# Optimization experiments

Measured on AMD Instinct MI355X. Metric: run time of the kernel, lower is better.

Reference implementation:

```python
import jax, jax.numpy as jnp
import numpy as np

N_HASHES = 4
CHUNK = 144
REDUCTION = 4
RES_SCALE = 0.1
L2_EPS = 5e-5


def _conv(x, w, b):
    # keras Conv2D, strides 1, padding 'same', NHWC/HWIO
    return jax.lax.conv_general_dilated(
        x, w, window_strides=(1, 1), padding='SAME',
        dimension_numbers=('NHWC', 'HWIO', 'NHWC')) + b


def setup_inputs() -> dict:
    key = jax.random.key(0)
    ks = jax.random.split(key, 4)
    N, H, W, Ch = 4, 96, 96, 256
    C = Ch // REDUCTION
    hb = min((H * W) // CHUNK + ((H * W) // CHUNK) % 2, 128)  # = 64
    return {
        'input': jax.random.normal(ks[0], (N, H, W, Ch), jnp.float32),
        'w_match': jax.random.normal(ks[1], (3, 3, Ch, C), jnp.float32) * 0.02,
        'b_match': jnp.zeros((C,), jnp.float32),
        'w_asm': jax.random.normal(ks[2], (3, 3, Ch, Ch), jnp.float32) * 0.02,
        'b_asm': jnp.zeros((Ch,), jnp.float32),
        'rotations': jax.random.normal(ks[3], (C, N_HASHES, hb // 2), jnp.float32),
    }


def reference(input, w_match, b_match, w_asm, b_asm, rotations):
    N, H, W, Ch = input.shape
    L = H * W
    C = Ch // REDUCTION
    nh = N_HASHES

    xm = _conv(input, w_match, b_match)   # (N,H,W,C)
    ya = _conv(input, w_asm, b_asm)       # (N,H,W,Ch)
    # Faithful to the TF code: reshape NHWC buffer to (N, C, L) then transpose.
    x_embed = xm.reshape(N, -1, L).transpose(0, 2, 1)  # (N, L, C)
    y_embed = ya.reshape(N, -1, L).transpose(0, 2, 1)  # (N, L, Ch)

    hash_buckets = min(L // CHUNK + (L // CHUNK) % 2, 128)
    # LSH: random rotations shared across batch
    rot = jnp.einsum('btf,fhi->bhti', x_embed, rotations)       # (N,nh,L,hb/2)
    rot = jnp.concatenate([rot, -rot], axis=-1)                 # (N,nh,L,hb)
    codes = jnp.argmax(rot, axis=-1).astype(jnp.int32)          # (N,nh,L)
    codes = codes + (jnp.arange(nh, dtype=jnp.int32) * hash_buckets)[None, :, None]
    codes = codes.reshape(N, -1)                                # (N, nh*L)

    idx = jnp.argsort(codes, axis=-1)
    undo_sort = jnp.argsort(idx, axis=-1)
    mod = idx % L

    xs = jnp.take_along_axis(x_embed, mod[..., None], axis=1)   # (N, nh*L, C)
    ys = jnp.take_along_axis(y_embed, mod[..., None], axis=1)   # (N, nh*L, Ch)

    pad = (CHUNK - L % CHUNK) % CHUNK
    xb = xs.reshape(N, nh, L, C)
    yb = ys.reshape(N, nh, L, Ch)
    if pad:
        xb = jnp.concatenate([xb, xb[:, :, -pad:]], axis=2)
        yb = jnp.concatenate([yb, yb[:, :, -pad:]], axis=2)
    xb = xb.reshape(N, nh, -1, CHUNK, C)    # (N,nh,K,chunk,C)
    yb = yb.reshape(N, nh, -1, CHUNK, Ch)

    # tf.math.l2_normalize: x * rsqrt(max(sum(x^2), eps))
    ss = jnp.sum(xb * xb, axis=-1, keepdims=True)
    x_match = xb * jax.lax.rsqrt(jnp.maximum(ss, L2_EPS))

    def add_adjacent(t):  # concat bucket, bucket-1, bucket+1 along chunk axis
        return jnp.concatenate(
            [t, jnp.roll(t, 1, axis=2), jnp.roll(t, -1, axis=2)], axis=3)

    x_match = add_adjacent(x_match)         # (N,nh,K,3*chunk,C)
    y3 = add_adjacent(yb)                   # (N,nh,K,3*chunk,Ch)

    raw = jnp.einsum('bhkie,bhkje->bhkij', xb, x_match)  # (N,nh,K,chunk,3chunk)
    lse = jax.scipy.special.logsumexp(raw, axis=-1, keepdims=True)
    score = jnp.exp(raw - lse)
    ret = jnp.einsum('bhkij,bhkje->bhkie', score, y3)    # (N,nh,K,chunk,Ch)

    ret = ret.reshape(N, nh, -1, Ch)
    bs = lse.reshape(N, nh, -1)
    if pad:
        ret = ret[:, :, :-pad]
        bs = bs[:, :, :-pad]

    ret = ret.reshape(N, nh * L, Ch)
    bs = bs.reshape(N, nh * L)
    ret = jnp.take_along_axis(ret, undo_sort[..., None], axis=1)
    bs = jnp.take_along_axis(bs, undo_sort, axis=1)

    ret = ret.reshape(N, nh, L, Ch)
    probs = jax.nn.softmax(bs.reshape(N, nh, L, 1), axis=1)
    ret = jnp.sum(ret * probs, axis=1)      # (N, L, Ch)

    ret = ret.transpose(0, 2, 1).reshape(N, H, W, Ch)  # inverse of the TF reshape
    return ret * RES_SCALE + input
```

## Files before the change

kernel.cpp:

```cpp
#include <hip/hip_runtime.h>
#include <cstdint>
#include <cstddef>

#define NB 4
#define HH 96
#define WW 96
#define CHN 256
#define CC 64
#define LL 9216
#define NHASH 4
#define HBK 64
#define CHK 144
#define NCHUNK 64
#define NJ 36864

typedef __attribute__((ext_vector_type(8))) short bf16x8;
typedef __attribute__((ext_vector_type(8))) unsigned short u16x8;
typedef __attribute__((ext_vector_type(4))) float f32x4;

__device__ __forceinline__ unsigned short f2b(float f) {
    unsigned int x = __float_as_uint(f);
    x += 0x7FFFu + ((x >> 16) & 1u);
    return (unsigned short)(x >> 16);
}
__device__ __forceinline__ float b2f(unsigned short u) {
    return __uint_as_float(((unsigned int)u) << 16);
}

__global__ __launch_bounds__(256) void cvt_in_hilo_k(const float* __restrict__ in,
                                                     unsigned short* __restrict__ hi,
                                                     unsigned short* __restrict__ lo)
{
    size_t g = ((size_t)blockIdx.x * 256 + threadIdx.x) * 8;
    float4 v0 = *(const float4*)(in + g);
    float4 v1 = *(const float4*)(in + g + 4);
    float xs[8] = {v0.x, v0.y, v0.z, v0.w, v1.x, v1.y, v1.z, v1.w};
    u16x8 h, l;
#pragma unroll
    for (int i = 0; i < 8; i++) {
        unsigned short hv = f2b(xs[i]);
        h[i] = hv;
        l[i] = f2b(xs[i] - b2f(hv));
    }
    *(u16x8*)(hi + g) = h;
    *(u16x8*)(lo + g) = l;
}

__global__ __launch_bounds__(256) void cvt_wm_hilo_k(const float* __restrict__ w,
                                                     unsigned short* __restrict__ hiT,
                                                     unsigned short* __restrict__ loT)
{
    __shared__ float tl[32][33];
    const int tap = blockIdx.z;
    const int c0 = blockIdx.x * 32;
    const int o0 = blockIdx.y * 32;
    const int tx = threadIdx.x & 31, ty0 = threadIdx.x >> 5;
#pragma unroll
    for (int i = 0; i < 32; i += 8)
        tl[ty0 + i][tx] = w[((size_t)tap * 256 + c0 + ty0 + i) * 64 + o0 + tx];
    __syncthreads();
#pragma unroll
    for (int i = 0; i < 32; i += 8) {
        float v = tl[tx][ty0 + i];
        unsigned short h = f2b(v);
        size_t o = ((size_t)tap * 64 + o0 + ty0 + i) * 256 + c0 + tx;
        hiT[o] = h;
        loT[o] = f2b(v - b2f(h));
    }
}

#define ASTR2 72
__global__ __launch_bounds__(256, 2) void conv_match_mfma_k(
    const unsigned short* __restrict__ in_hi, const unsigned short* __restrict__ in_lo,
    const unsigned short* __restrict__ wmT_hi, const unsigned short* __restrict__ wmT_lo,
    const float* __restrict__ bias, float* __restrict__ xm)
{
    __shared__ short Ah[64 * ASTR2], Al[64 * ASTR2];
    __shared__ short Bh[64 * ASTR2], Bl[64 * ASTR2];
    const int n = blockIdx.z, p0 = blockIdx.x * 64;
    const int tid = threadIdx.x;
    const int w = tid >> 6;
    const int lane = tid & 63, lm = lane & 15, lq = lane >> 4;
    const int r = tid >> 2, q8 = (tid & 3) * 8;
    const int p = p0 + r, py = p / WW, px = p % WW;
    const unsigned short* hiN = in_hi + (size_t)n * LL * CHN;
    const unsigned short* loN = in_lo + (size_t)n * LL * CHN;

    f32x4 acc[4];
#pragma unroll
    for (int b = 0; b < 4; b++) acc[b] = (f32x4){0.f, 0.f, 0.f, 0.f};

    u16x8 avh0 = (u16x8){0,0,0,0,0,0,0,0}, avh1 = (u16x8){0,0,0,0,0,0,0,0};
    u16x8 avl0 = (u16x8){0,0,0,0,0,0,0,0}, avl1 = (u16x8){0,0,0,0,0,0,0,0};
    u16x8 bvh0, bvh1, bvl0, bvl1;
    {
        int sy = py - 1, sx = px - 1;
        if (((unsigned)sy < HH) && ((unsigned)sx < WW)) {
            size_t ao = (size_t)(sy * WW + sx) * CHN + q8;
            avh0 = *(const u16x8*)(hiN + ao);
            avh1 = *(const u16x8*)(hiN + ao + 32);
            avl0 = *(const u16x8*)(loN + ao);
            avl1 = *(const u16x8*)(loN + ao + 32);
        }
        size_t bo = (size_t)r * 256 + q8;
        bvh0 = *(const u16x8*)(wmT_hi + bo);
        bvh1 = *(const u16x8*)(wmT_hi + bo + 32);
        bvl0 = *(const u16x8*)(wmT_lo + bo);
        bvl1 = *(const u16x8*)(wmT_lo + bo + 32);
    }

#pragma unroll 1
    for (int it = 0; it < 36; it++) {
        __syncthreads();
        *(u16x8*)&Ah[r * ASTR2 + q8]      = avh0;
        *(u16x8*)&Ah[r * ASTR2 + q8 + 32] = avh1;
        *(u16x8*)&Al[r * ASTR2 + q8]      = avl0;
        *(u16x8*)&Al[r * ASTR2 + q8 + 32] = avl1;
        *(u16x8*)&Bh[r * ASTR2 + q8]      = bvh0;
        *(u16x8*)&Bh[r * ASTR2 + q8 + 32] = bvh1;
        *(u16x8*)&Bl[r * ASTR2 + q8]      = bvl0;
        *(u16x8*)&Bl[r * ASTR2 + q8 + 32] = bvl1;
        if (it < 35) {
            int nit = it + 1;
            int ntap = nit >> 2, nci = (nit & 3) << 6;
            int ky = ntap / 3, kx = ntap - ky * 3;
            int sy = py + ky - 1, sx = px + kx - 1;
            avh0 = (u16x8){0,0,0,0,0,0,0,0}; avh1 = (u16x8){0,0,0,0,0,0,0,0};
            avl0 = (u16x8){0,0,0,0,0,0,0,0}; avl1 = (u16x8){0,0,0,0,0,0,0,0};
            if (((unsigned)sy < HH) && ((unsigned)sx < WW)) {
                size_t ao = (size_t)(sy * WW + sx) * CHN + q8 + nci;
                avh0 = *(const u16x8*)(hiN + ao);
                avh1 = *(const u16x8*)(hiN + ao + 32);
                avl0 = *(const u16x8*)(loN + ao);
                avl1 = *(const u16x8*)(loN + ao + 32);
            }
            size_t bo = ((size_t)ntap * 64 + r) * 256 + q8 + nci;
            bvh0 = *(const u16x8*)(wmT_hi + bo);
            bvh1 = *(const u16x8*)(wmT_hi + bo + 32);
            bvl0 = *(const u16x8*)(wmT_lo + bo);
            bvl1 = *(const u16x8*)(wmT_lo + bo + 32);
        }
        __syncthreads();
#pragma unroll
        for (int cs = 0; cs < 2; cs++) {
            bf16x8 afh = *(const bf16x8*)&Ah[(w * 16 + lm) * ASTR2 + cs * 32 + lq * 8];
            bf16x8 afl = *(const bf16x8*)&Al[(w * 16 + lm) * ASTR2 + cs * 32 + lq * 8];
#pragma unroll
            for (int nt = 0; nt < 4; nt++) {
                bf16x8 bfh = *(const bf16x8*)&Bh[(nt * 16 + lm) * ASTR2 + cs * 32 + lq * 8];
                bf16x8 bfl = *(const bf16x8*)&Bl[(nt * 16 + lm) * ASTR2 + cs * 32 + lq * 8];
                acc[nt] = __builtin_amdgcn_mfma_f32_16x16x32_bf16(afh, bfh, acc[nt], 0, 0, 0);
                acc[nt] = __builtin_amdgcn_mfma_f32_16x16x32_bf16(afh, bfl, acc[nt], 0, 0, 0);
                acc[nt] = __builtin_amdgcn_mfma_f32_16x16x32_bf16(afl, bfh, acc[nt], 0, 0, 0);
            }
        }
    }
    float bvv[4];
#pragma unroll
    for (int nt = 0; nt < 4; nt++) bvv[nt] = bias[nt * 16 + lm];
    float* outN = xm + (size_t)n * LL * 64;
#pragma unroll
    for (int r4 = 0; r4 < 4; r4++) {
        int row = p0 + w * 16 + lq * 4 + r4;
        float* od = outN + (size_t)row * 64;
#pragma unroll
        for (int nt = 0; nt < 4; nt++)
            od[nt * 16 + lm] = acc[nt][r4] + bvv[nt];
    }
}

__global__ __launch_bounds__(256) void transpose_k(const float* __restrict__ in, float* __restrict__ out,
                                                   unsigned short* __restrict__ out_bf, int R, int Cc)
{
    __shared__ float tl[32][33];
    const int n = blockIdx.z;
    const size_t base = (size_t)n * R * Cc;
    int c0 = blockIdx.x * 32, r0 = blockIdx.y * 32;
    int tx = threadIdx.x & 31, ty0 = threadIdx.x >> 5;
#pragma unroll
    for (int i = 0; i < 32; i += 8)
        tl[ty0 + i][tx] = in[base + (size_t)(r0 + ty0 + i) * Cc + c0 + tx];
    __syncthreads();
#pragma unroll
    for (int i = 0; i < 32; i += 8) {
        float v = tl[tx][ty0 + i];
        size_t o = base + (size_t)(c0 + ty0 + i) * R + r0 + tx;
        out[o] = v;
        out_bf[o] = f2b(v);
    }
}

__global__ __launch_bounds__(256) void cvt_wT_k(const float* __restrict__ w, unsigned short* __restrict__ wT)
{
    __shared__ float tl[32][33];
    const int tap = blockIdx.z;
    const int c0 = blockIdx.x * 32;
    const int o0 = blockIdx.y * 32;
    const int tx = threadIdx.x & 31, ty0 = threadIdx.x >> 5;
#pragma unroll
    for (int i = 0; i < 32; i += 8)
        tl[ty0 + i][tx] = w[((size_t)tap * 256 + c0 + ty0 + i) * 256 + o0 + tx];
    __syncthreads();
#pragma unroll
    for (int i = 0; i < 32; i += 8)
        wT[((size_t)tap * 256 + o0 + ty0 + i) * 256 + c0 + tx] = f2b(tl[tx][ty0 + i]);
}

__global__ __launch_bounds__(256) void conv_mfma_k(
    const unsigned short* __restrict__ in_bf, const unsigned short* __restrict__ wT,
    const float* __restrict__ bias, unsigned short* __restrict__ ya_bf)
{
    __shared__ short As[128 * ASTR2];
    __shared__ short Bs[128 * ASTR2];
    const int n = blockIdx.z, p0 = blockIdx.x * 128, co0 = blockIdx.y * 128;
    const int tid = threadIdx.x;
    const int w = tid >> 6, wr = w >> 1, wc = w & 1;
    const int lane = tid & 63, lm = lane & 15, lq = lane >> 4;
    const int r = tid >> 1, hf = tid & 1;
    const int p = p0 + r, py = p / WW, px = p % WW;
    const unsigned short* inN = in_bf + (size_t)n * LL * CHN;

    f32x4 acc[4][4];
#pragma unroll
    for (int a = 0; a < 4; a++)
#pragma unroll
        for (int b = 0; b < 4; b++) acc[a][b] = (f32x4){0.f, 0.f, 0.f, 0.f};

    u16x8 av0 = (u16x8){0,0,0,0,0,0,0,0}, av1 = (u16x8){0,0,0,0,0,0,0,0};
    u16x8 av2 = (u16x8){0,0,0,0,0,0,0,0}, av3 = (u16x8){0,0,0,0,0,0,0,0};
    u16x8 bv0, bv1, bv2, bv3;
    {
        int sy = py - 1, sx = px - 1;
        if (((unsigned)sy < HH) && ((unsigned)sx < WW)) {
            const unsigned short* asrc = inN + (size_t)(sy * WW + sx) * CHN + hf * 32;
            av0 = *(const u16x8*)(asrc);
            av1 = *(const u16x8*)(asrc + 8);
            av2 = *(const u16x8*)(asrc + 16);
            av3 = *(const u16x8*)(asrc + 24);
        }
        const unsigned short* bsrc = wT + ((size_t)co0 + r) * 256 + hf * 32;
        bv0 = *(const u16x8*)(bsrc);
        bv1 = *(const u16x8*)(bsrc + 8);
        bv2 = *(const u16x8*)(bsrc + 16);
        bv3 = *(const u16x8*)(bsrc + 24);
    }

#pragma unroll 1
    for (int it = 0; it < 36; it++) {
        __syncthreads();
        *(u16x8*)&As[r * ASTR2 + hf * 32]      = av0;
        *(u16x8*)&As[r * ASTR2 + hf * 32 + 8]  = av1;
        *(u16x8*)&As[r * ASTR2 + hf * 32 + 16] = av2;
        *(u16x8*)&As[r * ASTR2 + hf * 32 + 24] = av3;
        *(u16x8*)&Bs[r * ASTR2 + hf * 32]      = bv0;
        *(u16x8*)&Bs[r * ASTR2 + hf * 32 + 8]  = bv1;
        *(u16x8*)&Bs[r * ASTR2 + hf * 32 + 16] = bv2;
        *(u16x8*)&Bs[r * ASTR2 + hf * 32 + 24] = bv3;
        if (it < 35) {
            int nit = it + 1;
            int ntap = nit >> 2, nci = (nit & 3) << 6;
            int ky = ntap / 3, kx = ntap - ky * 3;
            int sy = py + ky - 1, sx = px + kx - 1;
            av0 = (u16x8){0,0,0,0,0,0,0,0}; av1 = (u16x8){0,0,0,0,0,0,0,0};
            av2 = (u16x8){0,0,0,0,0,0,0,0}; av3 = (u16x8){0,0,0,0,0,0,0,0};
            if (((unsigned)sy < HH) && ((unsigned)sx < WW)) {
                const unsigned short* asrc = inN + (size_t)(sy * WW + sx) * CHN + hf * 32 + nci;
                av0 = *(const u16x8*)(asrc);
                av1 = *(const u16x8*)(asrc + 8);
                av2 = *(const u16x8*)(asrc + 16);
                av3 = *(const u16x8*)(asrc + 24);
            }
            const unsigned short* bsrc = wT + ((size_t)ntap * 256 + co0 + r) * 256 + hf * 32 + nci;
            bv0 = *(const u16x8*)(bsrc);
            bv1 = *(const u16x8*)(bsrc + 8);
            bv2 = *(const u16x8*)(bsrc + 16);
            bv3 = *(const u16x8*)(bsrc + 24);
        }
        __syncthreads();
#pragma unroll
        for (int cs = 0; cs < 2; cs++) {
            bf16x8 af[4], bf[4];
#pragma unroll
            for (int mt = 0; mt < 4; mt++)
                af[mt] = *(const bf16x8*)&As[(wr * 64 + mt * 16 + lm) * ASTR2 + cs * 32 + lq * 8];
#pragma unroll
            for (int nt = 0; nt < 4; nt++)
                bf[nt] = *(const bf16x8*)&Bs[(wc * 64 + nt * 16 + lm) * ASTR2 + cs * 32 + lq * 8];
#pragma unroll
            for (int mt = 0; mt < 4; mt++)
#pragma unroll
                for (int nt = 0; nt < 4; nt++)
                    acc[mt][nt] = __builtin_amdgcn_mfma_f32_16x16x32_bf16(af[mt], bf[nt], acc[mt][nt], 0, 0, 0);
        }
    }
    float bv[4];
#pragma unroll
    for (int nt = 0; nt < 4; nt++) bv[nt] = bias[co0 + wc * 64 + nt * 16 + lm];
#pragma unroll
    for (int mt = 0; mt < 4; mt++) {
#pragma unroll
        for (int r4 = 0; r4 < 4; r4++) {
            int row = p0 + wr * 64 + mt * 16 + lq * 4 + r4;
            unsigned short* od = ya_bf + ((size_t)n * LL + row) * CHN + co0 + wc * 64;
#pragma unroll
            for (int nt = 0; nt < 4; nt++)
                od[nt * 16 + lm] = f2b(acc[mt][nt][r4] + bv[nt]);
        }
    }
}

__global__ __launch_bounds__(256) void transpose_bf_k(const unsigned short* __restrict__ in,
                                                      unsigned short* __restrict__ out)
{
    __shared__ unsigned short tl[64][65];
    const int n = blockIdx.z;
    const size_t base = (size_t)n * LL * CHN;
    const int t0 = blockIdx.x * 64, e0 = blockIdx.y * 64;
    const int tx = threadIdx.x & 63, ty0 = threadIdx.x >> 6;
#pragma unroll
    for (int i = 0; i < 16; i++) {
        int row = ty0 + i * 4;
        tl[row][tx] = in[base + (size_t)(e0 + row) * LL + t0 + tx];
    }
    __syncthreads();
#pragma unroll
    for (int i = 0; i < 16; i++) {
        int row = ty0 + i * 4;
        out[base + (size_t)(t0 + row) * CHN + e0 + tx] = tl[tx][row];
    }
}

__global__ __launch_bounds__(256) void hash_k(const float* __restrict__ xmT, const float* __restrict__ rot,
                                              int* __restrict__ codes, float* __restrict__ ssq)
{
    __shared__ float rs[32 * 68];
    const int h = blockIdx.y;
    for (int e = threadIdx.x; e < 2048; e += 256) {
        int hi = e >> 6, f = e & 63;
        rs[hi * 68 + f] = rot[f * 128 + h * 32 + hi];
    }
    __syncthreads();
    int g = blockIdx.x * 256 + threadIdx.x;
    int n = g / LL, t = g % LL;
    float4 x4[16];
    const float* src = xmT + (size_t)g * CC;
#pragma unroll
    for (int f4 = 0; f4 < 16; f4++) x4[f4] = *(const float4*)(src + f4 * 4);
    if (h == 0) {
        float ss = 0.f;
#pragma unroll
        for (int f4 = 0; f4 < 16; f4++)
            ss += x4[f4].x * x4[f4].x + x4[f4].y * x4[f4].y + x4[f4].z * x4[f4].z + x4[f4].w * x4[f4].w;
        ssq[g] = ss;
    }
    float bp = -1e30f, bn = -1e30f;
    int ip = 0, inn = 0;
    for (int i = 0; i < 32; i++) {
        const float* rr = &rs[i * 68];
        float d0 = 0.f, d1 = 0.f, d2 = 0.f, d3 = 0.f;
#pragma unroll
        for (int f4 = 0; f4 < 16; f4++) {
            float4 r4 = *(const float4*)(rr + f4 * 4);
            d0 = fmaf(x4[f4].x, r4.x, d0);
            d1 = fmaf(x4[f4].y, r4.y, d1);
            d2 = fmaf(x4[f4].z, r4.z, d2);
            d3 = fmaf(x4[f4].w, r4.w, d3);
        }
        float d = (d0 + d1) + (d2 + d3);
        if (d > bp) { bp = d; ip = i; }
        if (-d > bn) { bn = -d; inn = i; }
    }
    int code = (bp >= bn) ? ip : (32 + inn);
    codes[(size_t)n * NJ + h * LL + t] = code + h * HBK;
}

__global__ __launch_bounds__(256) void sort_hist_k(const int* __restrict__ codes, int* __restrict__ hist,
                                                   int* __restrict__ rank)
{
    __shared__ int lhw[4][256];
    const int n = blockIdx.y, seg = blockIdx.x, tid = threadIdx.x;
    const int w = tid >> 6, lane = tid & 63;
    int j = seg * 256 + tid;
    int c = codes[(size_t)n * NJ + j];
    for (int e = tid; e < 1024; e += 256) ((int*)lhw)[e] = 0;
    __syncthreads();
    unsigned long long eq = ~0ull;
#pragma unroll
    for (int b = 0; b < 8; b++) {
        unsigned long long m = __ballot((c >> b) & 1);
        eq &= ((c >> b) & 1) ? m : ~m;
    }
    int rw = __popcll(eq & ((1ull << lane) - 1ull));
    int cntw = __popcll(eq);
    if (rw == 0) lhw[w][c] = cntw;
    __syncthreads();
    int base = 0;
    if (w > 0) base += lhw[0][c];
    if (w > 1) base += lhw[1][c];
    if (w > 2) base += lhw[2][c];
    rank[(size_t)n * NJ + j] = base + rw;
    hist[(size_t)n * NJ + tid * 144 + seg] = lhw[0][tid] + lhw[1][tid] + lhw[2][tid] + lhw[3][tid];
}

__global__ __launch_bounds__(256) void sort_scan_k(int* __restrict__ hist)
{
    const int n = blockIdx.x;
    const int key = threadIdx.x;
    int* hn = hist + (size_t)n * NJ;
    int sum = 0;
    for (int s = 0; s < 144; s++) sum += hn[key * 144 + s];
    __shared__ int sc[256];
    sc[key] = sum;
    __syncthreads();
    for (int off = 1; off < 256; off <<= 1) {
        int v = (key >= off) ? sc[key - off] : 0;
        __syncthreads();
        sc[key] += v;
        __syncthreads();
    }
    int run = sc[key] - sum;
    for (int s = 0; s < 144; s++) { int v = hn[key * 144 + s]; hn[key * 144 + s] = run; run += v; }
}

__global__ __launch_bounds__(256) void sort_scatter_k(const int* __restrict__ codes, const int* __restrict__ rank,
                                                      const int* __restrict__ hist, int* __restrict__ sidx,
                                                      int* __restrict__ undo)
{
    const int n = blockIdx.y, seg = blockIdx.x, tid = threadIdx.x;
    int j = seg * 256 + tid;
    int c = codes[(size_t)n * NJ + j];
    int dest = hist[(size_t)n * NJ + c * 144 + seg] + rank[(size_t)n * NJ + j];
    sidx[(size_t)n * NJ + dest] = j;
    undo[(size_t)n * NJ + j] = dest;
}

#define QSTR 72
#define PSTR 164
__global__ __launch_bounds__(1024, 4) __attribute__((amdgpu_waves_per_eu(4, 4))) void attn_mfma_k(
    const unsigned short* __restrict__ xmT_bf, const unsigned short* __restrict__ yaT,
    const float* __restrict__ ssq, const int* __restrict__ sidx,
    unsigned short* __restrict__ Osort, float* __restrict__ bs)
{
    __shared__ short Qs[144 * QSTR];
    __shared__ short Ks[144 * QSTR];
    __shared__ short Ps[144 * PSTR];
    __shared__ int   tIdx[432];
    __shared__ int   voff[432];
    __shared__ float nfs[432];
    __shared__ float qlen[432];
    __shared__ float lsum[144];
    __shared__ float linv[144];

    const int k = blockIdx.x, h = blockIdx.y, n = blockIdx.z;
    const int tid = threadIdx.x;
    const int w = tid >> 6, lane = tid & 63;
    const int lm = lane & 15, lq = lane >> 4;
    const size_t sbase = (size_t)n * NJ + (size_t)h * LL;

    if (tid < 432) {
        int cc = tid / CHK, rr = tid - cc * CHK;
        int c = (cc == 0) ? k : (cc == 1 ? (k + NCHUNK - 1) & (NCHUNK - 1) : (k + 1) & (NCHUNK - 1));
        int j = sidx[sbase + c * CHK + rr];
        int t = j % LL;
        tIdx[tid] = t;
        voff[tid] = t * (CHN * 2);
        float m = fmaxf(ssq[(size_t)n * LL + t], 5e-5f);
        float nf = rsqrtf(m);
        nfs[tid] = nf;
        qlen[tid] = m * nf;
    }
    __syncthreads();

    const int sr = tid >> 3, sj = (tid & 7) * 8;
    const int sr2 = (tid + 1024) >> 3, sj2 = (tid & 7) * 8;
    {
        u16x8 v = *(const u16x8*)(xmT_bf + ((size_t)n * LL + tIdx[sr]) * CC + sj);
        *(u16x8*)&Qs[sr * QSTR + sj] = v;
        if (tid < 128) {
            u16x8 v2 = *(const u16x8*)(xmT_bf + ((size_t)n * LL + tIdx[sr2]) * CC + sj2);
            *(u16x8*)&Qs[sr2 * QSTR + sj2] = v2;
        }
    }
    for (int e = tid; e < 2304; e += 1024) {
        int r = e >> 4, c = 144 + (e & 15);
        Ps[r * PSTR + c] = 0;
    }
    u16x8 kreg0, kreg1;
    kreg0 = *(const u16x8*)(xmT_bf + ((size_t)n * LL + tIdx[CHK + sr]) * CC + sj);
    if (tid < 128)
        kreg1 = *(const u16x8*)(xmT_bf + ((size_t)n * LL + tIdx[CHK + sr2]) * CC + sj2);

    const char* vbase = (const char*)(yaT + (size_t)n * LL * CHN + w * 16 + lm);
    f32x4 accO[9];
#pragma unroll
    for (int mt = 0; mt < 9; mt++) accO[mt] = (f32x4){0.f, 0.f, 0.f, 0.f};
    f32x4 accL = (f32x4){0.f, 0.f, 0.f, 0.f};
    bf16x8 onesF, onesL;
#pragma unroll
    for (int i = 0; i < 8; i++) {
        onesF[i] = (short)0x3F80;
        onesL[i] = (lq < 2) ? (short)0x3F80 : (short)0;
    }

    for (int cc = 0; cc < 3; cc++) {
        const int c144 = cc * CHK;
        if (cc > 0) {
            *(u16x8*)&Ks[sr * QSTR + sj] = kreg0;
            if (tid < 128) *(u16x8*)&Ks[sr2 * QSTR + sj2] = kreg1;
        }
        if (cc < 2) {
            kreg0 = *(const u16x8*)(xmT_bf + ((size_t)n * LL + tIdx[(cc + 1) * CHK + sr]) * CC + sj);
            if (tid < 128)
                kreg1 = *(const u16x8*)(xmT_bf + ((size_t)n * LL + tIdx[(cc + 1) * CHK + sr2]) * CC + sj2);
        }
        bf16x8 vfrag[5];
#pragma unroll
        for (int ks = 0; ks < 5; ks++) {
            int kb = ks * 32 + lq * 8;
            if (kb < 144) {
                int4 o0 = *(const int4*)&voff[c144 + kb];
                int4 o1 = *(const int4*)&voff[c144 + kb + 4];
                vfrag[ks][0] = (short)*(const unsigned short*)(vbase + o0.x);
                vfrag[ks][1] = (short)*(const unsigned short*)(vbase + o0.y);
                vfrag[ks][2] = (short)*(const unsigned short*)(vbase + o0.z);
                vfrag[ks][3] = (short)*(const unsigned short*)(vbase + o0.w);
                vfrag[ks][4] = (short)*(const unsigned short*)(vbase + o1.x);
                vfrag[ks][5] = (short)*(const unsigned short*)(vbase + o1.y);
                vfrag[ks][6] = (short)*(const unsigned short*)(vbase + o1.z);
                vfrag[ks][7] = (short)*(const unsigned short*)(vbase + o1.w);
            } else {
                vfrag[ks] = (bf16x8){0, 0, 0, 0, 0, 0, 0, 0};
            }
        }
        __syncthreads();

        const short* Bsrc = (cc == 0) ? Qs : Ks;
        for (int tt = w; tt < 81; tt += 16) {
            int mt = tt / 9, nt = tt - mt * 9;
            f32x4 c = {0.f, 0.f, 0.f, 0.f};
#pragma unroll
            for (int ks = 0; ks < 2; ks++) {
                bf16x8 a = *(const bf16x8*)&Qs[(mt * 16 + lm) * QSTR + ks * 32 + lq * 8];
                bf16x8 b = *(const bf16x8*)&Bsrc[(nt * 16 + lm) * QSTR + ks * 32 + lq * 8];
                c = __builtin_amdgcn_mfma_f32_16x16x32_bf16(a, b, c, 0, 0, 0);
            }
            float nfk = nfs[c144 + nt * 16 + lm];
#pragma unroll
            for (int r = 0; r < 4; r++) {
                int mrow = mt * 16 + lq * 4 + r;
                float p = __expf(fmaf(c[r], nfk, -qlen[mrow]));
                Ps[mrow * PSTR + nt * 16 + lm] = (short)f2b(p);
            }
        }
        __syncthreads();

        if (w < 9) {
#pragma unroll
            for (int ks = 0; ks < 5; ks++) {
                bf16x8 a = *(const bf16x8*)&Ps[(w * 16 + lm) * PSTR + ks * 32 + lq * 8];
                accL = __builtin_amdgcn_mfma_f32_16x16x32_bf16(a, (ks == 4) ? onesL : onesF, accL, 0, 0, 0);
            }
        }
#pragma unroll
        for (int mt = 0; mt < 9; mt++) {
            f32x4 c = accO[mt];
#pragma unroll
            for (int ks = 0; ks < 5; ks++) {
                bf16x8 a = *(const bf16x8*)&Ps[(mt * 16 + lm) * PSTR + ks * 32 + lq * 8];
                c = __builtin_amdgcn_mfma_f32_16x16x32_bf16(a, vfrag[ks], c, 0, 0, 0);
            }
            accO[mt] = c;
        }
    }

    if (w < 9 && lm == 0) {
#pragma unroll
        for (int r = 0; r < 4; r++) lsum[w * 16 + lq * 4 + r] = accL[r];
    }
    __syncthreads();
    if (tid < 144) {
        float l = lsum[tid];
        linv[tid] = 1.0f / l;
        bs[sbase + tIdx[tid]] = qlen[tid] + __logf(l);
    }
    __syncthreads();

#pragma unroll
    for (int mt = 0; mt < 9; mt++) {
        f32x4 c = accO[mt];
#pragma unroll
        for (int r = 0; r < 4; r++) {
            int mrow = mt * 16 + lq * 4 + r;
            Osort[(sbase + (size_t)k * CHK + mrow) * CHN + w * 16 + lm] = f2b(c[r] * linv[mrow]);
        }
    }
}

__global__ __launch_bounds__(256) void combfin_k(
    const unsigned short* __restrict__ Osort, const float* __restrict__ bs,
    const int* __restrict__ undo, const float* __restrict__ inp, float* __restrict__ out)
{
    __shared__ float ac[32][260];
    __shared__ int   uS[4][32];
    __shared__ float pS[4][32];
    const int n = blockIdx.y;
    const int t0 = blockIdx.x * 32;
    const int tid = threadIdx.x;
    if (tid < 128) {
        int hh = tid >> 5, tt = tid & 31;
        size_t idx = (size_t)n * NJ + (size_t)hh * LL + t0 + tt;
        uS[hh][tt] = undo[idx];
        pS[hh][tt] = bs[idx];
    }
    __syncthreads();
    if (tid < 32) {
        float b0 = pS[0][tid], b1 = pS[1][tid], b2 = pS[2][tid], b3 = pS[3][tid];
        float mx = fmaxf(fmaxf(b0, b1), fmaxf(b2, b3));
        float e0 = __expf(b0 - mx), e1 = __expf(b1 - mx), e2 = __expf(b2 - mx), e3 = __expf(b3 - mx);
        float inv = 1.f / (e0 + e1 + e2 + e3);
        pS[0][tid] = e0 * inv; pS[1][tid] = e1 * inv; pS[2][tid] = e2 * inv; pS[3][tid] = e3 * inv;
    }
    __syncthreads();
    const int g = tid & 63, tq = tid >> 6;
    for (int tt8 = 0; tt8 < 8; tt8++) {
        int t = tq * 8 + tt8;
        float a0 = 0.f, a1 = 0.f, a2 = 0.f, a3 = 0.f;
#pragma unroll
        for (int hh = 0; hh < 4; hh++) {
            int row = uS[hh][t];
            float p = pS[hh][t];
            ushort4 u = *(const ushort4*)&Osort[((size_t)n * NJ + row) * CHN + g * 4];
            a0 = fmaf(p, b2f(u.x), a0);
            a1 = fmaf(p, b2f(u.y), a1);
            a2 = fmaf(p, b2f(u.z), a2);
            a3 = fmaf(p, b2f(u.w), a3);
        }
        *(float4*)&ac[t][g * 4] = make_float4(a0, a1, a2, a3);
    }
    __syncthreads();
    const int tp = tid & 31, er = tid >> 5;
    const float* inN = inp + (size_t)n * LL * CHN;
    float* outN = out + (size_t)n * LL * CHN;
    for (int it = 0; it < 32; it++) {
        int e = er + it * 8;
        size_t o = (size_t)e * LL + t0 + tp;
        outN[o] = ac[tp][e] * 0.1f + inN[o];
    }
}

extern "C" void kernel_launch(void* const* d_in, const int* in_sizes, int n_in,
                              void* d_out, int out_size, void* d_ws, size_t ws_size,
                              hipStream_t stream)
{
    (void)in_sizes; (void)n_in; (void)out_size; (void)ws_size;
    const float* input   = (const float*)d_in[0];
    const float* w_match = (const float*)d_in[1];
    const float* b_match = (const float*)d_in[2];
    const float* w_asm   = (const float*)d_in[3];
    const float* b_asm   = (const float*)d_in[4];
    const float* rot     = (const float*)d_in[5];
    float* out = (float*)d_out;

    char* ws = (char*)d_ws;
    size_t off = 0;
    auto alloc = [&](size_t bytes) -> void* {
        void* p = ws + off;
        off += (bytes + 255) & ~(size_t)255;
        return p;
    };
    unsigned short* in_bf  = (unsigned short*)alloc((size_t)NB * LL * CHN * 2);
    unsigned short* wT_bf  = (unsigned short*)alloc((size_t)9 * CHN * CHN * 2);
    unsigned short* ya_bf  = (unsigned short*)alloc((size_t)NB * LL * CHN * 2);
    unsigned short* yaT    = (unsigned short*)alloc((size_t)NB * LL * CHN * 2);
    float* xm     = (float*)alloc((size_t)NB * LL * CC * 4);
    float* xmT    = (float*)alloc((size_t)NB * LL * CC * 4);
    unsigned short* xmT_bf = (unsigned short*)alloc((size_t)NB * LL * CC * 2);
    float* ssq    = (float*)alloc((size_t)NB * LL * 4);
    int*   codes  = (int*)  alloc((size_t)NB * NJ * 4);
    int*   rank   = (int*)  alloc((size_t)NB * NJ * 4);
    int*   hist   = (int*)  alloc((size_t)NB * NJ * 4);
    int*   sidx   = (int*)  alloc((size_t)NB * NJ * 4);
    int*   undo   = (int*)  alloc((size_t)NB * NJ * 4);
    float* bs     = (float*)alloc((size_t)NB * NJ * 4);
    unsigned short* Osort = (unsigned short*)alloc((size_t)NB * NJ * CHN * 2);
    unsigned short* wmT_hi = (unsigned short*)alloc((size_t)9 * 64 * CHN * 2);
    unsigned short* wmT_lo = (unsigned short*)alloc((size_t)9 * 64 * CHN * 2);
    unsigned short* in_lo = Osort;

    cvt_in_hilo_k<<<dim3(4608), 256, 0, stream>>>(input, in_bf, in_lo);
    cvt_wm_hilo_k<<<dim3(8, 2, 9), 256, 0, stream>>>(w_match, wmT_hi, wmT_lo);
    conv_match_mfma_k<<<dim3(144, 1, NB), 256, 0, stream>>>(in_bf, in_lo, wmT_hi, wmT_lo, b_match, xm);
    transpose_k<<<dim3(288, 2, NB), 256, 0, stream>>>(xm, xmT, xmT_bf, CC, LL);
    cvt_wT_k<<<dim3(8, 8, 9), 256, 0, stream>>>(w_asm, wT_bf);
    conv_mfma_k<<<dim3(72, 2, NB), 256, 0, stream>>>(in_bf, wT_bf, b_asm, ya_bf);
    transpose_bf_k<<<dim3(144, 4, NB), 256, 0, stream>>>(ya_bf, yaT);
    hash_k<<<dim3(144, NHASH), 256, 0, stream>>>(xmT, rot, codes, ssq);
    sort_hist_k<<<dim3(144, NB), 256, 0, stream>>>(codes, hist, rank);
    sort_scan_k<<<dim3(NB), 256, 0, stream>>>(hist);
    sort_scatter_k<<<dim3(144, NB), 256, 0, stream>>>(codes, rank, hist, sidx, undo);
    attn_mfma_k<<<dim3(NCHUNK, NHASH, NB), 1024, 0, stream>>>(xmT_bf, yaT, ssq, sidx, Osort, bs);
    combfin_k<<<dim3(288, NB), 256, 0, stream>>>(Osort, bs, undo, input, out);
}
```

Baseline: 433.8 us.

## Merge independent conv, weight-convert and transpose kernels into combined launches

Combines the two weight-conversion kernels, the match and assembly convolutions, and the two transpose kernels into three launches that split work by block index. This cuts launch count and lets the small match-conv grid share the GPU with the larger assembly conv instead of running alone. In exchange, both branches share one shared-memory and register footprint and the launch bound of 2 blocks per CU. That may lower occupancy for the assembly-conv path, and the two branches have uneven block durations.

```diff
diff --git a/kernel.cpp b/kernel.cpp
--- a/kernel.cpp
+++ b/kernel.cpp
@@ -46,287 +46,291 @@
     *(u16x8*)(lo + g) = l;
 }
 
-__global__ __launch_bounds__(256) void cvt_wm_hilo_k(const float* __restrict__ w,
-                                                     unsigned short* __restrict__ hiT,
-                                                     unsigned short* __restrict__ loT)
+__global__ __launch_bounds__(256) void cvt_w_fused_k(const float* __restrict__ wm,
+                                                     unsigned short* __restrict__ wmT_hi,
+                                                     unsigned short* __restrict__ wmT_lo,
+                                                     const float* __restrict__ wa,
+                                                     unsigned short* __restrict__ wT)
 {
     __shared__ float tl[32][33];
     const int tap = blockIdx.z;
     const int c0 = blockIdx.x * 32;
-    const int o0 = blockIdx.y * 32;
     const int tx = threadIdx.x & 31, ty0 = threadIdx.x >> 5;
-#pragma unroll
-    for (int i = 0; i < 32; i += 8)
-        tl[ty0 + i][tx] = w[((size_t)tap * 256 + c0 + ty0 + i) * 64 + o0 + tx];
-    __syncthreads();
-#pragma unroll
-    for (int i = 0; i < 32; i += 8) {
-        float v = tl[tx][ty0 + i];
-        unsigned short h = f2b(v);
-        size_t o = ((size_t)tap * 64 + o0 + ty0 + i) * 256 + c0 + tx;
-        hiT[o] = h;
-        loT[o] = f2b(v - b2f(h));
+    if (blockIdx.y < 2) {
+        const int o0 = blockIdx.y * 32;
+#pragma unroll
+        for (int i = 0; i < 32; i += 8)
+            tl[ty0 + i][tx] = wm[((size_t)tap * 256 + c0 + ty0 + i) * 64 + o0 + tx];
+        __syncthreads();
+#pragma unroll
+        for (int i = 0; i < 32; i += 8) {
+            float v = tl[tx][ty0 + i];
+            unsigned short h = f2b(v);
+            size_t o = ((size_t)tap * 64 + o0 + ty0 + i) * 256 + c0 + tx;
+            wmT_hi[o] = h;
+            wmT_lo[o] = f2b(v - b2f(h));
+        }
+    } else {
+        const int o0 = (blockIdx.y - 2) * 32;
+#pragma unroll
+        for (int i = 0; i < 32; i += 8)
+            tl[ty0 + i][tx] = wa[((size_t)tap * 256 + c0 + ty0 + i) * 256 + o0 + tx];
+        __syncthreads();
+#pragma unroll
+        for (int i = 0; i < 32; i += 8)
+            wT[((size_t)tap * 256 + o0 + ty0 + i) * 256 + c0 + tx] = f2b(tl[tx][ty0 + i]);
     }
 }
 
 #define ASTR2 72
-__global__ __launch_bounds__(256, 2) void conv_match_mfma_k(
+__global__ __launch_bounds__(256, 2) void convs_fused_k(
     const unsigned short* __restrict__ in_hi, const unsigned short* __restrict__ in_lo,
     const unsigned short* __restrict__ wmT_hi, const unsigned short* __restrict__ wmT_lo,
-    const float* __restrict__ bias, float* __restrict__ xm)
-{
-    __shared__ short Ah[64 * ASTR2], Al[64 * ASTR2];
-    __shared__ short Bh[64 * ASTR2], Bl[64 * ASTR2];
-    const int n = blockIdx.z, p0 = blockIdx.x * 64;
+    const float* __restrict__ b_match, float* __restrict__ xm,
+    const unsigned short* __restrict__ wT, const float* __restrict__ b_asm,
+    unsigned short* __restrict__ ya_bf)
+{
+    __shared__ short smem[256 * ASTR2];
+    const int n = blockIdx.y;
     const int tid = threadIdx.x;
     const int w = tid >> 6;
     const int lane = tid & 63, lm = lane & 15, lq = lane >> 4;
-    const int r = tid >> 2, q8 = (tid & 3) * 8;
-    const int p = p0 + r, py = p / WW, px = p % WW;
-    const unsigned short* hiN = in_hi + (size_t)n * LL * CHN;
-    const unsigned short* loN = in_lo + (size_t)n * LL * CHN;
-
-    f32x4 acc[4];
-#pragma unroll
-    for (int b = 0; b < 4; b++) acc[b] = (f32x4){0.f, 0.f, 0.f, 0.f};
-
-    u16x8 avh0 = (u16x8){0,0,0,0,0,0,0,0}, avh1 = (u16x8){0,0,0,0,0,0,0,0};
-    u16x8 avl0 = (u16x8){0,0,0,0,0,0,0,0}, avl1 = (u16x8){0,0,0,0,0,0,0,0};
-    u16x8 bvh0, bvh1, bvl0, bvl1;
-    {
-        int sy = py - 1, sx = px - 1;
-        if (((unsigned)sy < HH) && ((unsigned)sx < WW)) {
-            size_t ao = (size_t)(sy * WW + sx) * CHN + q8;
-            avh0 = *(const u16x8*)(hiN + ao);
-            avh1 = *(const u16x8*)(hiN + ao + 32);
-            avl0 = *(const u16x8*)(loN + ao);
-            avl1 = *(const u16x8*)(loN + ao + 32);
-        }
-        size_t bo = (size_t)r * 256 + q8;
-        bvh0 = *(const u16x8*)(wmT_hi + bo);
-        bvh1 = *(const u16x8*)(wmT_hi + bo + 32);
-        bvl0 = *(const u16x8*)(wmT_lo + bo);
-        bvl1 = *(const u16x8*)(wmT_lo + bo + 32);
-    }
-
-#pragma unroll 1
-    for (int it = 0; it < 36; it++) {
-        __syncthreads();
-        *(u16x8*)&Ah[r * ASTR2 + q8]      = avh0;
-        *(u16x8*)&Ah[r * ASTR2 + q8 + 32] = avh1;
-        *(u16x8*)&Al[r * ASTR2 + q8]      = avl0;
-        *(u16x8*)&Al[r * ASTR2 + q8 + 32] = avl1;
-        *(u16x8*)&Bh[r * ASTR2 + q8]      = bvh0;
-        *(u16x8*)&Bh[r * ASTR2 + q8 + 32] = bvh1;
-        *(u16x8*)&Bl[r * ASTR2 + q8]      = bvl0;
-        *(u16x8*)&Bl[r * ASTR2 + q8 + 32] = bvl1;
-        if (it < 35) {
-            int nit = it + 1;
-            int ntap = nit >> 2, nci = (nit & 3) << 6;
-            int ky = ntap / 3, kx = ntap - ky * 3;
-            int sy = py + ky - 1, sx = px + kx - 1;
-            avh0 = (u16x8){0,0,0,0,0,0,0,0}; avh1 = (u16x8){0,0,0,0,0,0,0,0};
-            avl0 = (u16x8){0,0,0,0,0,0,0,0}; avl1 = (u16x8){0,0,0,0,0,0,0,0};
+
+    if (blockIdx.x < 144) {
+        short* Ah = smem;
+        short* Al = smem + 64 * ASTR2;
+        short* Bh = smem + 128 * ASTR2;
+        short* Bl = smem + 192 * ASTR2;
+        const int p0 = blockIdx.x * 64;
+        const int r = tid >> 2, q8 = (tid & 3) * 8;
+        const int p = p0 + r, py = p / WW, px = p % WW;
+        const unsigned short* hiN = in_hi + (size_t)n * LL * CHN;
+        const unsigned short* loN = in_lo + (size_t)n * LL * CHN;
+
+        f32x4 acc[4];
+#pragma unroll
+        for (int b = 0; b < 4; b++) acc[b] = (f32x4){0.f, 0.f, 0.f, 0.f};
+
+        u16x8 avh0 = (u16x8){0,0,0,0,0,0,0,0}, avh1 = (u16x8){0,0,0,0,0,0,0,0};
+        u16x8 avl0 = (u16x8){0,0,0,0,0,0,0,0}, avl1 = (u16x8){0,0,0,0,0,0,0,0};
+        u16x8 bvh0, bvh1, bvl0, bvl1;
+        {
+            int sy = py - 1, sx = px - 1;
             if (((unsigned)sy < HH) && ((unsigned)sx < WW)) {
-                size_t ao = (size_t)(sy * WW + sx) * CHN + q8 + nci;
+                size_t ao = (size_t)(sy * WW + sx) * CHN + q8;
                 avh0 = *(const u16x8*)(hiN + ao);
                 avh1 = *(const u16x8*)(hiN + ao + 32);
                 avl0 = *(const u16x8*)(loN + ao);
                 avl1 = *(const u16x8*)(loN + ao + 32);
             }
-            size_t bo = ((size_t)ntap * 64 + r) * 256 + q8 + nci;
+            size_t bo = (size_t)r * 256 + q8;
             bvh0 = *(const u16x8*)(wmT_hi + bo);
             bvh1 = *(const u16x8*)(wmT_hi + bo + 32);
             bvl0 = *(const u16x8*)(wmT_lo + bo);
             bvl1 = *(const u16x8*)(wmT_lo + bo + 32);
         }
-        __syncthreads();
-#pragma unroll
-        for (int cs = 0; cs < 2; cs++) {
-            bf16x8 afh = *(const bf16x8*)&Ah[(w * 16 + lm) * ASTR2 + cs * 32 + lq * 8];
-            bf16x8 afl = *(const bf16x8*)&Al[(w * 16 + lm) * ASTR2 + cs * 32 + lq * 8];
-#pragma unroll
-            for (int nt = 0; nt < 4; nt++) {
-                bf16x8 bfh = *(const bf16x8*)&Bh[(nt * 16 + lm) * ASTR2 + cs * 32 + lq * 8];
-                bf16x8 bfl = *(const bf16x8*)&Bl[(nt * 16 + lm) * ASTR2 + cs * 32 + lq * 8];
-                acc[nt] = __builtin_amdgcn_mfma_f32_16x16x32_bf16(afh, bfh, acc[nt], 0, 0, 0);
-                acc[nt] = __builtin_amdgcn_mfma_f32_16x16x32_bf16(afh, bfl, acc[nt], 0, 0, 0);
-                acc[nt] = __builtin_amdgcn_mfma_f32_16x16x32_bf16(afl, bfh, acc[nt], 0, 0, 0);
-            }
-        }
-    }
-    float bvv[4];
-#pragma unroll
-    for (int nt = 0; nt < 4; nt++) bvv[nt] = bias[nt * 16 + lm];
-    float* outN = xm + (size_t)n * LL * 64;
-#pragma unroll
-    for (int r4 = 0; r4 < 4; r4++) {
-        int row = p0 + w * 16 + lq * 4 + r4;
-        float* od = outN + (size_t)row * 64;
-#pragma unroll
-        for (int nt = 0; nt < 4; nt++)
-            od[nt * 16 + lm] = acc[nt][r4] + bvv[nt];
-    }
-}
-
-__global__ __launch_bounds__(256) void transpose_k(const float* __restrict__ in, float* __restrict__ out,
-                                                   unsigned short* __restrict__ out_bf, int R, int Cc)
-{
-    __shared__ float tl[32][33];
-    const int n = blockIdx.z;
-    const size_t base = (size_t)n * R * Cc;
-    int c0 = blockIdx.x * 32, r0 = blockIdx.y * 32;
-    int tx = threadIdx.x & 31, ty0 = threadIdx.x >> 5;
-#pragma unroll
-    for (int i = 0; i < 32; i += 8)
-        tl[ty0 + i][tx] = in[base + (size_t)(r0 + ty0 + i) * Cc + c0 + tx];
-    __syncthreads();
-#pragma unroll
-    for (int i = 0; i < 32; i += 8) {
-        float v = tl[tx][ty0 + i];
-        size_t o = base + (size_t)(c0 + ty0 + i) * R + r0 + tx;
-        out[o] = v;
-        out_bf[o] = f2b(v);
-    }
-}
-
-__global__ __launch_bounds__(256) void cvt_wT_k(const float* __restrict__ w, unsigned short* __restrict__ wT)
-{
-    __shared__ float tl[32][33];
-    const int tap = blockIdx.z;
-    const int c0 = blockIdx.x * 32;
-    const int o0 = blockIdx.y * 32;
-    const int tx = threadIdx.x & 31, ty0 = threadIdx.x >> 5;
-#pragma unroll
-    for (int i = 0; i < 32; i += 8)
-        tl[ty0 + i][tx] = w[((size_t)tap * 256 + c0 + ty0 + i) * 256 + o0 + tx];
-    __syncthreads();
-#pragma unroll
-    for (int i = 0; i < 32; i += 8)
-        wT[((size_t)tap * 256 + o0 + ty0 + i) * 256 + c0 + tx] = f2b(tl[tx][ty0 + i]);
-}
-
-__global__ __launch_bounds__(256) void conv_mfma_k(
-    const unsigned short* __restrict__ in_bf, const unsigned short* __restrict__ wT,
-    const float* __restrict__ bias, unsigned short* __restrict__ ya_bf)
-{
-    __shared__ short As[128 * ASTR2];
-    __shared__ short Bs[128 * ASTR2];
-    const int n = blockIdx.z, p0 = blockIdx.x * 128, co0 = blockIdx.y * 128;
-    const int tid = threadIdx.x;
-    const int w = tid >> 6, wr = w >> 1, wc = w & 1;
-    const int lane = tid & 63, lm = lane & 15, lq = lane >> 4;
-    const int r = tid >> 1, hf = tid & 1;
-    const int p = p0 + r, py = p / WW, px = p % WW;
-    const unsigned short* inN = in_bf + (size_t)n * LL * CHN;
-
-    f32x4 acc[4][4];
-#pragma unroll
-    for (int a = 0; a < 4; a++)
-#pragma unroll
-        for (int b = 0; b < 4; b++) acc[a][b] = (f32x4){0.f, 0.f, 0.f, 0.f};
-
-    u16x8 av0 = (u16x8){0,0,0,0,0,0,0,0}, av1 = (u16x8){0,0,0,0,0,0,0,0};
-    u16x8 av2 = (u16x8){0,0,0,0,0,0,0,0}, av3 = (u16x8){0,0,0,0,0,0,0,0};
-    u16x8 bv0, bv1, bv2, bv3;
-    {
-        int sy = py - 1, sx = px - 1;
-        if (((unsigned)sy < HH) && ((unsigned)sx < WW)) {
-            const unsigned short* asrc = inN + (size_t)(sy * WW + sx) * CHN + hf * 32;
-            av0 = *(const u16x8*)(asrc);
-            av1 = *(const u16x8*)(asrc + 8);
-            av2 = *(const u16x8*)(asrc + 16);
-            av3 = *(const u16x8*)(asrc + 24);
-        }
-        const unsigned short* bsrc = wT + ((size_t)co0 + r) * 256 + hf * 32;
-        bv0 = *(const u16x8*)(bsrc);
-        bv1 = *(const u16x8*)(bsrc + 8);
-        bv2 = *(const u16x8*)(bsrc + 16);
-        bv3 = *(const u16x8*)(bsrc + 24);
-    }
 
 #pragma unroll 1
-    for (int it = 0; it < 36; it++) {
-        __syncthreads();
-        *(u16x8*)&As[r * ASTR2 + hf * 32]      = av0;
-        *(u16x8*)&As[r * ASTR2 + hf * 32 + 8]  = av1;
-        *(u16x8*)&As[r * ASTR2 + hf * 32 + 16] = av2;
-        *(u16x8*)&As[r * ASTR2 + hf * 32 + 24] = av3;
-        *(u16x8*)&Bs[r * ASTR2 + hf * 32]      = bv0;
-        *(u16x8*)&Bs[r * ASTR2 + hf * 32 + 8]  = bv1;
-        *(u16x8*)&Bs[r * ASTR2 + hf * 32 + 16] = bv2;
-        *(u16x8*)&Bs[r * ASTR2 + hf * 32 + 24] = bv3;
-        if (it < 35) {
-            int nit = it + 1;
-            int ntap = nit >> 2, nci = (nit & 3) << 6;
-            int ky = ntap / 3, kx = ntap - ky * 3;
-            int sy = py + ky - 1, sx = px + kx - 1;
-            av0 = (u16x8){0,0,0,0,0,0,0,0}; av1 = (u16x8){0,0,0,0,0,0,0,0};
-            av2 = (u16x8){0,0,0,0,0,0,0,0}; av3 = (u16x8){0,0,0,0,0,0,0,0};
+        for (int it = 0; it < 36; it++) {
+            __syncthreads();
+            *(u16x8*)&Ah[r * ASTR2 + q8]      = avh0;
+            *(u16x8*)&Ah[r * ASTR2 + q8 + 32] = avh1;
+            *(u16x8*)&Al[r * ASTR2 + q8]      = avl0;
+            *(u16x8*)&Al[r * ASTR2 + q8 + 32] = avl1;
+            *(u16x8*)&Bh[r * ASTR2 + q8]      = bvh0;
+            *(u16x8*)&Bh[r * ASTR2 + q8 + 32] = bvh1;
+            *(u16x8*)&Bl[r * ASTR2 + q8]      = bvl0;
+            *(u16x8*)&Bl[r * ASTR2 + q8 + 32] = bvl1;
+            if (it < 35) {
+                int nit = it + 1;
+                int ntap = nit >> 2, nci = (nit & 3) << 6;
+                int ky = ntap / 3, kx = ntap - ky * 3;
+                int sy = py + ky - 1, sx = px + kx - 1;
+                avh0 = (u16x8){0,0,0,0,0,0,0,0}; avh1 = (u16x8){0,0,0,0,0,0,0,0};
+                avl0 = (u16x8){0,0,0,0,0,0,0,0}; avl1 = (u16x8){0,0,0,0,0,0,0,0};
+                if (((unsigned)sy < HH) && ((unsigned)sx < WW)) {
+                    size_t ao = (size_t)(sy * WW + sx) * CHN + q8 + nci;
+                    avh0 = *(const u16x8*)(hiN + ao);
+                    avh1 = *(const u16x8*)(hiN + ao + 32);
+                    avl0 = *(const u16x8*)(loN + ao);
+                    avl1 = *(const u16x8*)(loN + ao + 32);
+                }
+                size_t bo = ((size_t)ntap * 64 + r) * 256 + q8 + nci;
+                bvh0 = *(const u16x8*)(wmT_hi + bo);
+                bvh1 = *(const u16x8*)(wmT_hi + bo + 32);
+                bvl0 = *(const u16x8*)(wmT_lo + bo);
+                bvl1 = *(const u16x8*)(wmT_lo + bo + 32);
+            }
+            __syncthreads();
+#pragma unroll
+            for (int cs = 0; cs < 2; cs++) {
+                bf16x8 afh = *(const bf16x8*)&Ah[(w * 16 + lm) * ASTR2 + cs * 32 + lq * 8];
+                bf16x8 afl = *(const bf16x8*)&Al[(w * 16 + lm) * ASTR2 + cs * 32 + lq * 8];
+#pragma unroll
+                for (int nt = 0; nt < 4; nt++) {
+                    bf16x8 bfh = *(const bf16x8*)&Bh[(nt * 16 + lm) * ASTR2 + cs * 32 + lq * 8];
+                    bf16x8 bfl = *(const bf16x8*)&Bl[(nt * 16 + lm) * ASTR2 + cs * 32 + lq * 8];
+                    acc[nt] = __builtin_amdgcn_mfma_f32_16x16x32_bf16(afh, bfh, acc[nt], 0, 0, 0);
+                    acc[nt] = __builtin_amdgcn_mfma_f32_16x16x32_bf16(afh, bfl, acc[nt], 0, 0, 0);
+                    acc[nt] = __builtin_amdgcn_mfma_f32_16x16x32_bf16(afl, bfh, acc[nt], 0, 0, 0);
+                }
+            }
+        }
+        float bvv[4];
+#pragma unroll
+        for (int nt = 0; nt < 4; nt++) bvv[nt] = b_match[nt * 16 + lm];
+        float* outN = xm + (size_t)n * LL * 64;
+#pragma unroll
+        for (int r4 = 0; r4 < 4; r4++) {
+            int row = p0 + w * 16 + lq * 4 + r4;
+            float* od = outN + (size_t)row * 64;
+#pragma unroll
+            for (int nt = 0; nt < 4; nt++)
+                od[nt * 16 + lm] = acc[nt][r4] + bvv[nt];
+        }
+    } else {
+        short* As = smem;
+        short* Bs = smem + 128 * ASTR2;
+        const int idx = blockIdx.x - 144;
+        const int co_blk = idx / 72;
+        const int px_blk = idx - co_blk * 72;
+        const int p0 = px_blk * 128, co0 = co_blk * 128;
+        const int wr = w >> 1, wc = w & 1;
+        const int r = tid >> 1, hf = tid & 1;
+        const int p = p0 + r, py = p / WW, px = p % WW;
+        const unsigned short* inN = in_hi + (size_t)n * LL * CHN;
+
+        f32x4 acc[4][4];
+#pragma unroll
+        for (int a = 0; a < 4; a++)
+#pragma unroll
+            for (int b = 0; b < 4; b++) acc[a][b] = (f32x4){0.f, 0.f, 0.f, 0.f};
+
+        u16x8 av0 = (u16x8){0,0,0,0,0,0,0,0}, av1 = (u16x8){0,0,0,0,0,0,0,0};
+        u16x8 av2 = (u16x8){0,0,0,0,0,0,0,0}, av3 = (u16x8){0,0,0,0,0,0,0,0};
+        u16x8 bv0, bv1, bv2, bv3;
+        {
+            int sy = py - 1, sx = px - 1;
             if (((unsigned)sy < HH) && ((unsigned)sx < WW)) {
-                const unsigned short* asrc = inN + (size_t)(sy * WW + sx) * CHN + hf * 32 + nci;
+                const unsigned short* asrc = inN + (size_t)(sy * WW + sx) * CHN + hf * 32;
                 av0 = *(const u16x8*)(asrc);
                 av1 = *(const u16x8*)(asrc + 8);
                 av2 = *(const u16x8*)(asrc + 16);
                 av3 = *(const u16x8*)(asrc + 24);
             }
-            const unsigned short* bsrc = wT + ((size_t)ntap * 256 + co0 + r) * 256 + hf * 32 + nci;
+            const unsigned short* bsrc = wT + ((size_t)co0 + r) * 256 + hf * 32;
             bv0 = *(const u16x8*)(bsrc);
             bv1 = *(const u16x8*)(bsrc + 8);
             bv2 = *(const u16x8*)(bsrc + 16);
             bv3 = *(const u16x8*)(bsrc + 24);
         }
+
+#pragma unroll 1
+        for (int it = 0; it < 36; it++) {
+            __syncthreads();
+            *(u16x8*)&As[r * ASTR2 + hf * 32]      = av0;
+            *(u16x8*)&As[r * ASTR2 + hf * 32 + 8]  = av1;
+            *(u16x8*)&As[r * ASTR2 + hf * 32 + 16] = av2;
+            *(u16x8*)&As[r * ASTR2 + hf * 32 + 24] = av3;
+            *(u16x8*)&Bs[r * ASTR2 + hf * 32]      = bv0;
+            *(u16x8*)&Bs[r * ASTR2 + hf * 32 + 8]  = bv1;
+            *(u16x8*)&Bs[r * ASTR2 + hf * 32 + 16] = bv2;
+            *(u16x8*)&Bs[r * ASTR2 + hf * 32 + 24] = bv3;
+            if (it < 35) {
+                int nit = it + 1;
+                int ntap = nit >> 2, nci = (nit & 3) << 6;
+                int ky = ntap / 3, kx = ntap - ky * 3;
+                int sy = py + ky - 1, sx = px + kx - 1;
+                av0 = (u16x8){0,0,0,0,0,0,0,0}; av1 = (u16x8){0,0,0,0,0,0,0,0};
+                av2 = (u16x8){0,0,0,0,0,0,0,0}; av3 = (u16x8){0,0,0,0,0,0,0,0};
+                if (((unsigned)sy < HH) && ((unsigned)sx < WW)) {
+                    const unsigned short* asrc = inN + (size_t)(sy * WW + sx) * CHN + hf * 32 + nci;
+                    av0 = *(const u16x8*)(asrc);
+                    av1 = *(const u16x8*)(asrc + 8);
+                    av2 = *(const u16x8*)(asrc + 16);
+                    av3 = *(const u16x8*)(asrc + 24);
+                }
+                const unsigned short* bsrc = wT + ((size_t)ntap * 256 + co0 + r) * 256 + hf * 32 + nci;
+                bv0 = *(const u16x8*)(bsrc);
+                bv1 = *(const u16x8*)(bsrc + 8);
+                bv2 = *(const u16x8*)(bsrc + 16);
+                bv3 = *(const u16x8*)(bsrc + 24);
+            }
+            __syncthreads();
+#pragma unroll
+            for (int cs = 0; cs < 2; cs++) {
+                bf16x8 af[4], bf[4];
+#pragma unroll
+                for (int mt = 0; mt < 4; mt++)
+                    af[mt] = *(const bf16x8*)&As[(wr * 64 + mt * 16 + lm) * ASTR2 + cs * 32 + lq * 8];
+#pragma unroll
+                for (int nt = 0; nt < 4; nt++)
+                    bf[nt] = *(const bf16x8*)&Bs[(wc * 64 + nt * 16 + lm) * ASTR2 + cs * 32 + lq * 8];
+#pragma unroll
+                for (int mt = 0; mt < 4; mt++)
+#pragma unroll
+                    for (int nt = 0; nt < 4; nt++)
+                        acc[mt][nt] = __builtin_amdgcn_mfma_f32_16x16x32_bf16(af[mt], bf[nt], acc[mt][nt], 0, 0, 0);
+            }
+        }
+        float bv[4];
+#pragma unroll
+        for (int nt = 0; nt < 4; nt++) bv[nt] = b_asm[co0 + wc * 64 + nt * 16 + lm];
+#pragma unroll
+        for (int mt = 0; mt < 4; mt++) {
+#pragma unroll
+            for (int r4 = 0; r4 < 4; r4++) {
+                int row = p0 + wr * 64 + mt * 16 + lq * 4 + r4;
+                unsigned short* od = ya_bf + ((size_t)n * LL + row) * CHN + co0 + wc * 64;
+#pragma unroll
+                for (int nt = 0; nt < 4; nt++)
+                    od[nt * 16 + lm] = f2b(acc[mt][nt][r4] + bv[nt]);
+            }
+        }
+    }
+}
+
+__global__ __launch_bounds__(256) void transposes_fused_k(
+    const float* __restrict__ xm, float* __restrict__ xmT, unsigned short* __restrict__ xmT_bf,
+    const unsigned short* __restrict__ ya_bf, unsigned short* __restrict__ yaT)
+{
+    __shared__ float tlf[32][33];
+    __shared__ unsigned short tlb[64][65];
+    const int n = blockIdx.y;
+    if (blockIdx.x < 576) {
+        const int idx = blockIdx.x;
+        const int by = idx / 288, bx = idx - by * 288;
+        const size_t base = (size_t)n * 64 * LL;
+        const int c0 = bx * 32, r0 = by * 32;
+        const int tx = threadIdx.x & 31, ty0 = threadIdx.x >> 5;
+#pragma unroll
+        for (int i = 0; i < 32; i += 8)
+            tlf[ty0 + i][tx] = xm[base + (size_t)(r0 + ty0 + i) * LL + c0 + tx];
         __syncthreads();
 #pragma unroll
-        for (int cs = 0; cs < 2; cs++) {
-            bf16x8 af[4], bf[4];
-#pragma unroll
-            for (int mt = 0; mt < 4; mt++)
-                af[mt] = *(const bf16x8*)&As[(wr * 64 + mt * 16 + lm) * ASTR2 + cs * 32 + lq * 8];
-#pragma unroll
-            for (int nt = 0; nt < 4; nt++)
-                bf[nt] = *(const bf16x8*)&Bs[(wc * 64 + nt * 16 + lm) * ASTR2 + cs * 32 + lq * 8];
-#pragma unroll
-            for (int mt = 0; mt < 4; mt++)
-#pragma unroll
-                for (int nt = 0; nt < 4; nt++)
-                    acc[mt][nt] = __builtin_amdgcn_mfma_f32_16x16x32_bf16(af[mt], bf[nt], acc[mt][nt], 0, 0, 0);
-        }
-    }
-    float bv[4];
-#pragma unroll
-    for (int nt = 0; nt < 4; nt++) bv[nt] = bias[co0 + wc * 64 + nt * 16 + lm];
-#pragma unroll
-    for (int mt = 0; mt < 4; mt++) {
-#pragma unroll
-        for (int r4 = 0; r4 < 4; r4++) {
-            int row = p0 + wr * 64 + mt * 16 + lq * 4 + r4;
-            unsigned short* od = ya_bf + ((size_t)n * LL + row) * CHN + co0 + wc * 64;
-#pragma unroll
-            for (int nt = 0; nt < 4; nt++)
-                od[nt * 16 + lm] = f2b(acc[mt][nt][r4] + bv[nt]);
-        }
-    }
-}
-
-__global__ __launch_bounds__(256) void transpose_bf_k(const unsigned short* __restrict__ in,
-                                                      unsigned short* __restrict__ out)
-{
-    __shared__ unsigned short tl[64][65];
-    const int n = blockIdx.z;
-    const size_t base = (size_t)n * LL * CHN;
-    const int t0 = blockIdx.x * 64, e0 = blockIdx.y * 64;
-    const int tx = threadIdx.x & 63, ty0 = threadIdx.x >> 6;
-#pragma unroll
-    for (int i = 0; i < 16; i++) {
-        int row = ty0 + i * 4;
-        tl[row][tx] = in[base + (size_t)(e0 + row) * LL + t0 + tx];
-    }
-    __syncthreads();
-#pragma unroll
-    for (int i = 0; i < 16; i++) {
-        int row = ty0 + i * 4;
-        out[base + (size_t)(t0 + row) * CHN + e0 + tx] = tl[tx][row];
+        for (int i = 0; i < 32; i += 8) {
+            float v = tlf[tx][ty0 + i];
+            size_t o = base + (size_t)(c0 + ty0 + i) * 64 + r0 + tx;
+            xmT[o] = v;
+            xmT_bf[o] = f2b(v);
+        }
+    } else {
+        const int idx = blockIdx.x - 576;
+        const int by = idx / 144, bx = idx - by * 144;
+        const size_t base = (size_t)n * LL * CHN;
+        const int t0 = bx * 64, e0 = by * 64;
+        const int tx = threadIdx.x & 63, ty0 = threadIdx.x >> 6;
+#pragma unroll
+        for (int i = 0; i < 16; i++) {
+            int row = ty0 + i * 4;
+            tlb[row][tx] = ya_bf[base + (size_t)(e0 + row) * LL + t0 + tx];
+        }
+        __syncthreads();
+#pragma unroll
+        for (int i = 0; i < 16; i++) {
+            int row = ty0 + i * 4;
+            yaT[base + (size_t)(t0 + row) * CHN + e0 + tx] = tlb[tx][row];
+        }
     }
 }
 
@@ -688,12 +692,10 @@
     unsigned short* in_lo = Osort;
 
     cvt_in_hilo_k<<<dim3(4608), 256, 0, stream>>>(input, in_bf, in_lo);
-    cvt_wm_hilo_k<<<dim3(8, 2, 9), 256, 0, stream>>>(w_match, wmT_hi, wmT_lo);
-    conv_match_mfma_k<<<dim3(144, 1, NB), 256, 0, stream>>>(in_bf, in_lo, wmT_hi, wmT_lo, b_match, xm);
-    transpose_k<<<dim3(288, 2, NB), 256, 0, stream>>>(xm, xmT, xmT_bf, CC, LL);
-    cvt_wT_k<<<dim3(8, 8, 9), 256, 0, stream>>>(w_asm, wT_bf);
-    conv_mfma_k<<<dim3(72, 2, NB), 256, 0, stream>>>(in_bf, wT_bf, b_asm, ya_bf);
-    transpose_bf_k<<<dim3(144, 4, NB), 256, 0, stream>>>(ya_bf, yaT);
+    cvt_w_fused_k<<<dim3(8, 10, 9), 256, 0, stream>>>(w_match, wmT_hi, wmT_lo, w_asm, wT_bf);
+    convs_fused_k<<<dim3(288, NB), 256, 0, stream>>>(in_bf, in_lo, wmT_hi, wmT_lo, b_match, xm,
+                                                     wT_bf, b_asm, ya_bf);
+    transposes_fused_k<<<dim3(1152, NB), 256, 0, stream>>>(xm, xmT, xmT_bf, ya_bf, yaT);
     hash_k<<<dim3(144, NHASH), 256, 0, stream>>>(xmT, rot, codes, ssq);
     sort_hist_k<<<dim3(144, NB), 256, 0, stream>>>(codes, hist, rank);
     sort_scan_k<<<dim3(NB), 256, 0, stream>>>(hist);
```

Measured after the change: 397.6 us. 8.4% less time.
